# Optimization experiments

Measured on AMD Instinct MI355X. Metric: run time of the kernel, lower is better.

Reference implementation:

```python
import jax, jax.numpy as jnp
import numpy as np

B, S, H, NH = 2, 2048, 1024, 16
HD = H // NH  # 64


def setup_inputs() -> dict:
    key = jax.random.key(0)
    ks = jax.random.split(key, 9)
    s = 1.0 / np.sqrt(H)
    d = {"x": jax.random.normal(ks[0], (B, S, H), jnp.float32)}
    for i, n in enumerate(["Wq", "Wk", "Wv", "Wo"]):
        d[n] = jax.random.normal(ks[1 + i], (H, H), jnp.float32) * s
    for i, n in enumerate(["bq", "bk", "bv", "bo"]):
        d[n] = jax.random.normal(ks[5 + i], (H,), jnp.float32) * s
    return d


def _heads(x, W, b):
    # torch nn.Linear: y = x @ W.T + b, then split heads -> (B, NH, S, HD)
    y = x @ W.T + b
    return y.reshape(B, S, NH, HD).transpose(0, 2, 1, 3)


def _tetra_channels(t):
    # tetrapoint vector [a, 1-a, a*(1-a), clamp(1-(a+(1-a)),0,1)] for a scalar slice t
    a = jax.nn.sigmoid(t)
    na = 1.0 - a
    neither = jnp.clip(1.0 - (a + na), 0.0, 1.0)
    return jnp.stack([a, na, a * na, neither], axis=-1)  # (..., 4)


def reference(x, Wq, bq, Wk, bk, Wv, bv, Wo, bo):
    Q = _heads(x, Wq, bq)  # (B, NH, S, HD)
    K = _heads(x, Wk, bk)
    V = _heads(x, Wv, bv)
    # Original indexes Q_tetrapoints[:, :, :, 0] on [B,NH,S,HD,4]: selects head-dim
    # slot 0 (resp. 2) and keeps the 4 tetrapoint channels -> (B, NH, S, 4).
    Qa = _tetra_channels(Q[..., 0])
    Ka = _tetra_channels(K[..., 0])
    Qb = _tetra_channels(Q[..., 2])
    Kb = _tetra_channels(K[..., 2])
    scores = (jnp.einsum('bhsc,bhtc->bhst', Qa, Ka) / np.sqrt(HD)
              + 0.1 * jnp.einsum('bhsc,bhtc->bhst', Qb, Kb))  # (B, NH, S, S)
    w = jax.nn.softmax(scores, axis=-1)
    out = jnp.einsum('bhst,bhtd->bhsd', w, V)  # (B, NH, S, HD)
    out = out.transpose(0, 2, 1, 3).reshape(B, S, H)
    return out @ Wo.T + bo
```

## Files before the change

kernel.cpp:

```cpp
#include <hip/hip_runtime.h>
#include <hip/hip_bf16.h>

#define SS 2048
#define HH 1024
#define NHH 16
#define HDD 64

using f32x4  = __attribute__((ext_vector_type(4))) float;
using bf16x8 = __attribute__((ext_vector_type(8))) short;

__device__ __forceinline__ unsigned short f2bf(float f) {
    unsigned u = __builtin_bit_cast(unsigned, f);
    unsigned r = u + 0x7FFFu + ((u >> 16) & 1u);
    return (unsigned short)(r >> 16);
}

__device__ __forceinline__ unsigned bfround(float f) {
    unsigned u = __builtin_bit_cast(unsigned, f);
    return u + 0x7FFFu + ((u >> 16) & 1u);
}
__device__ __forceinline__ unsigned pack2bf(float a, float b) {
    return __builtin_amdgcn_perm(bfround(b), bfround(a), 0x07060302u);
}

__device__ __forceinline__ void tetra(float t, float* c) {
    float a = 1.f / (1.f + __expf(-t));
    float na = 1.f - a;
    float nei = 1.f - (a + na);
    nei = fminf(fmaxf(nei, 0.f), 1.f);
    c[0] = a; c[1] = na; c[2] = a * na; c[3] = nei;
}

__global__ __launch_bounds__(256) void cvt_kernel(
    const float* __restrict__ x, const float* __restrict__ Wv, const float* __restrict__ Wo,
    const float* __restrict__ Wq, const float* __restrict__ Wk,
    const float* __restrict__ bq, const float* __restrict__ bk,
    unsigned short* __restrict__ xb, unsigned short* __restrict__ Wvb, unsigned short* __restrict__ Wob,
    unsigned short* __restrict__ wselb, float* __restrict__ bselws)
{
    if (blockIdx.x >= 2048) {
        int n = blockIdx.x - 2048;
        int h = n >> 2, q = n & 3;
        int rowIdx = h * HDD + ((q & 1) ? 2 : 0);
        const float* src  = (q & 2) ? Wk : Wq;
        const float* bsrc = (q & 2) ? bk : bq;
        int t = threadIdx.x;
        float4 v = *(const float4*)(src + (size_t)rowIdx * HH + t * 4);
        uint2 pk;
        pk.x = pack2bf(v.x, v.y);
        pk.y = pack2bf(v.z, v.w);
        *(uint2*)(wselb + (size_t)n * HH + t * 4) = pk;
        if (t == 0) bselws[n] = bsrc[rowIdx];
        return;
    }
    size_t gid = (size_t)blockIdx.x * 256 + threadIdx.x;
    size_t base = gid * 8;
    {
        float4 a = *(const float4*)(x + base);
        float4 b = *(const float4*)(x + base + 4);
        uint4 pk;
        pk.x = pack2bf(a.x, a.y);
        pk.y = pack2bf(a.z, a.w);
        pk.z = pack2bf(b.x, b.y);
        pk.w = pack2bf(b.z, b.w);
        *(uint4*)(xb + base) = pk;
    }
    if (base < 1048576) {
        float4 a = *(const float4*)(Wv + base);
        float4 b = *(const float4*)(Wv + base + 4);
        uint4 pk;
        pk.x = pack2bf(a.x, a.y);
        pk.y = pack2bf(a.z, a.w);
        pk.z = pack2bf(b.x, b.y);
        pk.w = pack2bf(b.z, b.w);
        *(uint4*)(Wvb + base) = pk;
        a = *(const float4*)(Wo + base);
        b = *(const float4*)(Wo + base + 4);
        pk.x = pack2bf(a.x, a.y);
        pk.y = pack2bf(a.z, a.w);
        pk.z = pack2bf(b.x, b.y);
        pk.w = pack2bf(b.z, b.w);
        *(uint4*)(Wob + base) = pk;
    }
}

__global__ __launch_bounds__(256) void qk_gemm_kernel(
    const unsigned short* __restrict__ xb, const unsigned short* __restrict__ wselb,
    const float* __restrict__ bselws,
    unsigned short* __restrict__ qfb, unsigned short* __restrict__ kfb)
{
    __shared__ unsigned short xs[32][72];
    __shared__ unsigned short ws[64][72];
    __shared__ float ys[32][68];
    int tid = threadIdx.x;
    int wave = tid >> 6, lane = tid & 63;
    int l15 = lane & 15, l16 = lane >> 4;
    int m0 = blockIdx.x * 32;
    int n0w = wave * 16;

    int xr = tid >> 3, xseg = (tid & 7) * 8;
    int wr = tid >> 2, wseg = (tid & 3) * 16;
    const unsigned short* xp = xb + (size_t)(m0 + xr) * HH + xseg;
    const unsigned short* wp = wselb + (size_t)wr * HH + wseg;

    f32x4 acc[2] = {};

    uint4 xv  = *(const uint4*)(xp);
    uint4 wv0 = *(const uint4*)(wp);
    uint4 wv1 = *(const uint4*)(wp + 8);

    for (int k0 = 0; k0 < HH; k0 += 64) {
        __syncthreads();
        *(uint4*)&xs[xr][xseg] = xv;
        *(uint4*)&ws[wr][wseg]     = wv0;
        *(uint4*)&ws[wr][wseg + 8] = wv1;
        __syncthreads();

        int kn = (k0 + 64) & (HH - 1);
        uint4 nxv  = *(const uint4*)(xp + kn);
        uint4 nwv0 = *(const uint4*)(wp + kn);
        uint4 nwv1 = *(const uint4*)(wp + kn + 8);

        #pragma unroll
        for (int kk = 0; kk < 64; kk += 32) {
            bf16x8 bfr = *(const bf16x8*)&ws[n0w + l15][kk + l16 * 8];
            #pragma unroll
            for (int mi = 0; mi < 2; mi++) {
                bf16x8 af = *(const bf16x8*)&xs[mi * 16 + l15][kk + l16 * 8];
                acc[mi] = __builtin_amdgcn_mfma_f32_16x16x32_bf16(af, bfr, acc[mi], 0, 0, 0);
            }
        }
        xv = nxv; wv0 = nwv0; wv1 = nwv1;
    }

    float bias = bselws[n0w + l15];
    __syncthreads();
    #pragma unroll
    for (int mi = 0; mi < 2; mi++)
        #pragma unroll
        for (int r = 0; r < 4; r++)
            ys[mi * 16 + l16 * 4 + r][n0w + l15] = acc[mi][r] + bias;
    __syncthreads();

    #pragma unroll
    for (int pass = 0; pass < 2; pass++) {
        int ml = tid & 31;
        int h = (tid >> 5) + pass * 8;
        float4 y4 = *(const float4*)&ys[ml][h * 4];
        float qa[4], qb2[4], ka[4], kb2[4];
        tetra(y4.x, qa);
        tetra(y4.y, qb2);
        tetra(y4.z, ka);
        tetra(y4.w, kb2);
        int m = m0 + ml, b = m >> 11, s = m & 2047;
        size_t base = ((size_t)(b * NHH + h) * SS + s) * 8;
        uint4 qp, kp;
        qp.x = pack2bf(qa[0] * 0.125f, qa[1] * 0.125f);
        qp.y = pack2bf(qa[2] * 0.125f, qa[3] * 0.125f);
        qp.z = pack2bf(qb2[0] * 0.1f, qb2[1] * 0.1f);
        qp.w = pack2bf(qb2[2] * 0.1f, qb2[3] * 0.1f);
        kp.x = pack2bf(ka[0], ka[1]);
        kp.y = pack2bf(ka[2], ka[3]);
        kp.z = pack2bf(kb2[0], kb2[1]);
        kp.w = pack2bf(kb2[2], kb2[3]);
        *(uint4*)(qfb + base) = qp;
        *(uint4*)(kfb + base) = kp;
    }
}

template<int OUT_MODE>
__global__ __launch_bounds__(256) void gemm_mfma(
    const unsigned short* __restrict__ A, const unsigned short* __restrict__ Bw,
    const float* __restrict__ bias, void* __restrict__ Cout)
{
    __shared__ unsigned short As[128][72];
    __shared__ unsigned short Bs[64][72];
    int tid = threadIdx.x;
    int wave = tid >> 6, lane = tid & 63;
    int l15 = lane & 15, l16 = lane >> 4;
    int wm = wave >> 1, wn = wave & 1;
    int m0 = blockIdx.y * 128, n0 = blockIdx.x * 64;

    int ar = tid >> 1, aseg = (tid & 1) * 32;
    int br = tid >> 2, bseg = (tid & 3) * 16;
    const unsigned short* Ap = A + (size_t)(m0 + ar) * HH + aseg;
    const unsigned short* Bp = Bw + (size_t)(n0 + br) * HH + bseg;

    f32x4 acc[4][2] = {};

    uint4 a0 = *(const uint4*)(Ap);
    uint4 a1 = *(const uint4*)(Ap + 8);
    uint4 a2 = *(const uint4*)(Ap + 16);
    uint4 a3 = *(const uint4*)(Ap + 24);
    uint4 b0 = *(const uint4*)(Bp);
    uint4 b1 = *(const uint4*)(Bp + 8);

    for (int k0 = 0; k0 < HH; k0 += 64) {
        __syncthreads();
        *(uint4*)&As[ar][aseg]      = a0;
        *(uint4*)&As[ar][aseg + 8]  = a1;
        *(uint4*)&As[ar][aseg + 16] = a2;
        *(uint4*)&As[ar][aseg + 24] = a3;
        *(uint4*)&Bs[br][bseg]      = b0;
        *(uint4*)&Bs[br][bseg + 8]  = b1;
        __syncthreads();

        int kn = (k0 + 64) & (HH - 1);
        uint4 na0 = *(const uint4*)(Ap + kn);
        uint4 na1 = *(const uint4*)(Ap + kn + 8);
        uint4 na2 = *(const uint4*)(Ap + kn + 16);
        uint4 na3 = *(const uint4*)(Ap + kn + 24);
        uint4 nb0 = *(const uint4*)(Bp + kn);
        uint4 nb1 = *(const uint4*)(Bp + kn + 8);

        #pragma unroll
        for (int kk = 0; kk < 64; kk += 32) {
            bf16x8 af[4], bfr[2];
            #pragma unroll
            for (int mi = 0; mi < 4; mi++)
                af[mi] = *(const bf16x8*)&As[wm * 64 + mi * 16 + l15][kk + l16 * 8];
            #pragma unroll
            for (int ni = 0; ni < 2; ni++)
                bfr[ni] = *(const bf16x8*)&Bs[wn * 32 + ni * 16 + l15][kk + l16 * 8];
            #pragma unroll
            for (int mi = 0; mi < 4; mi++)
                #pragma unroll
                for (int ni = 0; ni < 2; ni++)
                    acc[mi][ni] = __builtin_amdgcn_mfma_f32_16x16x32_bf16(af[mi], bfr[ni], acc[mi][ni], 0, 0, 0);
        }
        a0 = na0; a1 = na1; a2 = na2; a3 = na3; b0 = nb0; b1 = nb1;
    }

    float bv[2];
    #pragma unroll
    for (int ni = 0; ni < 2; ni++)
        bv[ni] = bias[n0 + wn * 32 + ni * 16 + l15];

    #pragma unroll
    for (int mi = 0; mi < 4; mi++) {
        #pragma unroll
        for (int ni = 0; ni < 2; ni++) {
            int n = n0 + wn * 32 + ni * 16 + l15;
            if (OUT_MODE == 0) {
                #pragma unroll
                for (int r = 0; r < 4; r++) {
                    int m = m0 + wm * 64 + mi * 16 + l16 * 4 + r;
                    ((float*)Cout)[(size_t)m * HH + n] = acc[mi][ni][r] + bv[ni];
                }
            } else {
                int m = m0 + wm * 64 + mi * 16 + l16 * 4;
                int b = m >> 11, s = m & 2047;
                int h = n >> 6, d = n & 63;
                uint2 pk;
                pk.x = pack2bf(acc[mi][ni][0] + bv[ni], acc[mi][ni][1] + bv[ni]);
                pk.y = pack2bf(acc[mi][ni][2] + bv[ni], acc[mi][ni][3] + bv[ni]);
                *(uint2*)((unsigned short*)Cout + ((size_t)((b * NHH + h) * HDD + d)) * SS + s) = pk;
            }
        }
    }
}

__global__ __launch_bounds__(256) void attn_mfma(
    const unsigned short* __restrict__ qfb, const unsigned short* __restrict__ kfb,
    const unsigned short* __restrict__ Vt, unsigned short* __restrict__ attnb)
{
    __shared__ unsigned short vt[64][72];
    __shared__ unsigned short ps[4][16][72];

    int tid = threadIdx.x;
    int wave = tid >> 6, lane = tid & 63;
    int l15 = lane & 15, l16 = lane >> 4;
    int bh = blockIdx.y, b = bh >> 4, h = bh & 15;
    int s0 = blockIdx.x * 64 + wave * 16;

    bf16x8 bfq = {0,0,0,0,0,0,0,0};
    if (l16 == 0)
        bfq = *(const bf16x8*)(qfb + ((size_t)bh * SS + s0 + l15) * 8);

    const short oneb = 0x3F80;
    bf16x8 ones = {oneb,oneb,oneb,oneb,oneb,oneb,oneb,oneb};

    const unsigned short* kfA = kfb + ((size_t)bh * SS + l15) * 8;
    int vd = tid >> 2, vseg = (tid & 3) * 16;
    const unsigned short* vsrc = Vt + ((size_t)bh * HDD + vd) * SS + vseg;

    f32x4 acc[4] = {};
    f32x4 accl = {};

    uint4 sv0 = *(const uint4*)(vsrc);
    uint4 sv1 = *(const uint4*)(vsrc + 8);
    bf16x8 kfr[4];
    #pragma unroll
    for (int tb = 0; tb < 4; tb++)
        kfr[tb] = *(const bf16x8*)(kfA + (size_t)(tb * 16) * 8);

    for (int t0 = 0; t0 < SS; t0 += 64) {
        __syncthreads();
        *(uint4*)&vt[vd][vseg]     = sv0;
        *(uint4*)&vt[vd][vseg + 8] = sv1;
        __syncthreads();

        int tn = (t0 + 64) & (SS - 1);
        uint4 nv0 = *(const uint4*)(vsrc + tn);
        uint4 nv1 = *(const uint4*)(vsrc + tn + 8);
        bf16x8 nkf[4];
        #pragma unroll
        for (int tb = 0; tb < 4; tb++)
            nkf[tb] = *(const bf16x8*)(kfA + (size_t)(tn + tb * 16) * 8);

        #pragma unroll
        for (int tb = 0; tb < 4; tb++) {
            f32x4 sc = {};
            sc = __builtin_amdgcn_mfma_f32_16x16x32_bf16(kfr[tb], bfq, sc, 0, 0, 0);
            float p0 = __expf(sc[0]);
            float p1 = __expf(sc[1]);
            float p2 = __expf(sc[2]);
            float p3 = __expf(sc[3]);
            uint2 pw;
            pw.x = pack2bf(p0, p1);
            pw.y = pack2bf(p2, p3);
            *(uint2*)&ps[wave][l15][tb * 16 + l16 * 4] = pw;
        }

        #pragma unroll
        for (int tk = 0; tk < 2; tk++) {
            bf16x8 ap = *(const bf16x8*)&ps[wave][l15][tk * 32 + l16 * 8];
            accl = __builtin_amdgcn_mfma_f32_16x16x32_bf16(ap, ones, accl, 0, 0, 0);
            #pragma unroll
            for (int nd = 0; nd < 4; nd++) {
                bf16x8 bv = *(const bf16x8*)&vt[nd * 16 + l15][tk * 32 + l16 * 8];
                acc[nd] = __builtin_amdgcn_mfma_f32_16x16x32_bf16(ap, bv, acc[nd], 0, 0, 0);
            }
        }

        sv0 = nv0; sv1 = nv1;
        #pragma unroll
        for (int tb = 0; tb < 4; tb++) kfr[tb] = nkf[tb];
    }

    #pragma unroll
    for (int r = 0; r < 4; r++) {
        float linv = 1.f / accl[r];
        int q = s0 + l16 * 4 + r;
        size_t row = (size_t)(b * SS + q) * HH + h * HDD;
        #pragma unroll
        for (int nd = 0; nd < 4; nd++)
            attnb[row + nd * 16 + l15] = f2bf(acc[nd][r] * linv);
    }
}

extern "C" void kernel_launch(void* const* d_in, const int* in_sizes, int n_in,
                              void* d_out, int out_size, void* d_ws, size_t ws_size,
                              hipStream_t stream)
{
    const float* x  = (const float*)d_in[0];
    const float* Wq = (const float*)d_in[1];
    const float* Wk = (const float*)d_in[2];
    const float* Wv = (const float*)d_in[3];
    const float* Wo = (const float*)d_in[4];
    const float* bq = (const float*)d_in[5];
    const float* bk = (const float*)d_in[6];
    const float* bv = (const float*)d_in[7];
    const float* bo = (const float*)d_in[8];

    unsigned short* qfb   = (unsigned short*)d_ws;
    unsigned short* kfb   = qfb + 524288;
    unsigned short* xb    = kfb + 524288;
    unsigned short* attnb = xb;
    unsigned short* Wvb   = xb + 4194304;
    unsigned short* Wob   = Wvb + 1048576;
    unsigned short* Vt    = Wob + 1048576;
    unsigned short* wselb  = Vt + 4194304;
    float*          bselws = (float*)(wselb + 65536);

    cvt_kernel<<<2112, 256, 0, stream>>>(x, Wv, Wo, Wq, Wk, bq, bk, xb, Wvb, Wob, wselb, bselws);
    qk_gemm_kernel<<<128, 256, 0, stream>>>(xb, wselb, bselws, qfb, kfb);
    gemm_mfma<2><<<dim3(16, 32), 256, 0, stream>>>(xb, Wvb, bv, Vt);
    attn_mfma<<<dim3(32, 32), 256, 0, stream>>>(qfb, kfb, Vt, attnb);
    gemm_mfma<0><<<dim3(16, 32), 256, 0, stream>>>(attnb, Wob, bo, (float*)d_out);
}
```

Measured before the change: 185.2 us.

## Process two query tiles per wave in attention and use exp2 with prescaled Q

The attention block shrinks from four waves to two, and each wave now handles 32 query rows as two 16-row groups. Each K fragment and V tile read from shared memory is reused across both groups, which halves the K global loads and the V LDS reads per query. The Q scale factors are multiplied by log2(e) so the softmax can use the hardware exp2 instead of __expf. Register pressure rises and each block has fewer waves to hide latency.

```diff
diff --git a/kernel.cpp b/kernel.cpp
--- a/kernel.cpp
+++ b/kernel.cpp
@@ -8,6 +8,12 @@
 
 using f32x4  = __attribute__((ext_vector_type(4))) float;
 using bf16x8 = __attribute__((ext_vector_type(8))) short;
+
+#if __has_builtin(__builtin_amdgcn_exp2f)
+#define EXP2F __builtin_amdgcn_exp2f
+#else
+#define EXP2F exp2f
+#endif
 
 __device__ __forceinline__ unsigned short f2bf(float f) {
     unsigned u = __builtin_bit_cast(unsigned, f);
@@ -154,11 +160,13 @@
         tetra(y4.w, kb2);
         int m = m0 + ml, b = m >> 11, s = m & 2047;
         size_t base = ((size_t)(b * NHH + h) * SS + s) * 8;
+        const float sA = 0.18033688011112042f;
+        const float sB = 0.14426950408889634f;
         uint4 qp, kp;
-        qp.x = pack2bf(qa[0] * 0.125f, qa[1] * 0.125f);
-        qp.y = pack2bf(qa[2] * 0.125f, qa[3] * 0.125f);
-        qp.z = pack2bf(qb2[0] * 0.1f, qb2[1] * 0.1f);
-        qp.w = pack2bf(qb2[2] * 0.1f, qb2[3] * 0.1f);
+        qp.x = pack2bf(qa[0] * sA, qa[1] * sA);
+        qp.y = pack2bf(qa[2] * sA, qa[3] * sA);
+        qp.z = pack2bf(qb2[0] * sB, qb2[1] * sB);
+        qp.w = pack2bf(qb2[2] * sB, qb2[3] * sB);
         kp.x = pack2bf(ka[0], ka[1]);
         kp.y = pack2bf(ka[2], ka[3]);
         kp.z = pack2bf(kb2[0], kb2[1]);
@@ -260,35 +268,39 @@
     }
 }
 
-__global__ __launch_bounds__(256) void attn_mfma(
+__global__ __launch_bounds__(128) void attn_mfma(
     const unsigned short* __restrict__ qfb, const unsigned short* __restrict__ kfb,
     const unsigned short* __restrict__ Vt, unsigned short* __restrict__ attnb)
 {
     __shared__ unsigned short vt[64][72];
-    __shared__ unsigned short ps[4][16][72];
+    __shared__ unsigned short ps[2][32][72];
 
     int tid = threadIdx.x;
     int wave = tid >> 6, lane = tid & 63;
     int l15 = lane & 15, l16 = lane >> 4;
     int bh = blockIdx.y, b = bh >> 4, h = bh & 15;
-    int s0 = blockIdx.x * 64 + wave * 16;
-
-    bf16x8 bfq = {0,0,0,0,0,0,0,0};
-    if (l16 == 0)
-        bfq = *(const bf16x8*)(qfb + ((size_t)bh * SS + s0 + l15) * 8);
+    int s0 = blockIdx.x * 64 + wave * 32;
+
+    bf16x8 bfq0 = {0,0,0,0,0,0,0,0};
+    bf16x8 bfq1 = {0,0,0,0,0,0,0,0};
+    if (l16 == 0) {
+        bfq0 = *(const bf16x8*)(qfb + ((size_t)bh * SS + s0 + l15) * 8);
+        bfq1 = *(const bf16x8*)(qfb + ((size_t)bh * SS + s0 + 16 + l15) * 8);
+    }
 
     const short oneb = 0x3F80;
     bf16x8 ones = {oneb,oneb,oneb,oneb,oneb,oneb,oneb,oneb};
 
     const unsigned short* kfA = kfb + ((size_t)bh * SS + l15) * 8;
-    int vd = tid >> 2, vseg = (tid & 3) * 16;
+    int vd = tid >> 1, vseg = (tid & 1) * 32;
     const unsigned short* vsrc = Vt + ((size_t)bh * HDD + vd) * SS + vseg;
 
-    f32x4 acc[4] = {};
-    f32x4 accl = {};
-
-    uint4 sv0 = *(const uint4*)(vsrc);
-    uint4 sv1 = *(const uint4*)(vsrc + 8);
+    f32x4 acc[2][4] = {};
+    f32x4 accl[2] = {};
+
+    uint4 sv[4];
+    #pragma unroll
+    for (int j = 0; j < 4; j++) sv[j] = *(const uint4*)(vsrc + j * 8);
     bf16x8 kfr[4];
     #pragma unroll
     for (int tb = 0; tb < 4; tb++)
@@ -296,13 +308,15 @@
 
     for (int t0 = 0; t0 < SS; t0 += 64) {
         __syncthreads();
-        *(uint4*)&vt[vd][vseg]     = sv0;
-        *(uint4*)&vt[vd][vseg + 8] = sv1;
+        #pragma unroll
+        for (int j = 0; j < 4; j++)
+            *(uint4*)&vt[vd][vseg + j * 8] = sv[j];
         __syncthreads();
 
         int tn = (t0 + 64) & (SS - 1);
-        uint4 nv0 = *(const uint4*)(vsrc + tn);
-        uint4 nv1 = *(const uint4*)(vsrc + tn + 8);
+        uint4 nv[4];
+        #pragma unroll
+        for (int j = 0; j < 4; j++) nv[j] = *(const uint4*)(vsrc + tn + j * 8);
         bf16x8 nkf[4];
         #pragma unroll
         for (int tb = 0; tb < 4; tb++)
@@ -310,42 +324,55 @@
 
         #pragma unroll
         for (int tb = 0; tb < 4; tb++) {
-            f32x4 sc = {};
-            sc = __builtin_amdgcn_mfma_f32_16x16x32_bf16(kfr[tb], bfq, sc, 0, 0, 0);
-            float p0 = __expf(sc[0]);
-            float p1 = __expf(sc[1]);
-            float p2 = __expf(sc[2]);
-            float p3 = __expf(sc[3]);
-            uint2 pw;
-            pw.x = pack2bf(p0, p1);
-            pw.y = pack2bf(p2, p3);
-            *(uint2*)&ps[wave][l15][tb * 16 + l16 * 4] = pw;
+            #pragma unroll
+            for (int qg = 0; qg < 2; qg++) {
+                f32x4 sc = {};
+                sc = __builtin_amdgcn_mfma_f32_16x16x32_bf16(kfr[tb], qg ? bfq1 : bfq0, sc, 0, 0, 0);
+                float p0 = EXP2F(sc[0]);
+                float p1 = EXP2F(sc[1]);
+                float p2 = EXP2F(sc[2]);
+                float p3 = EXP2F(sc[3]);
+                uint2 pw;
+                pw.x = pack2bf(p0, p1);
+                pw.y = pack2bf(p2, p3);
+                *(uint2*)&ps[wave][qg * 16 + l15][tb * 16 + l16 * 4] = pw;
+            }
         }
 
         #pragma unroll
         for (int tk = 0; tk < 2; tk++) {
-            bf16x8 ap = *(const bf16x8*)&ps[wave][l15][tk * 32 + l16 * 8];
-            accl = __builtin_amdgcn_mfma_f32_16x16x32_bf16(ap, ones, accl, 0, 0, 0);
+            bf16x8 ap[2];
+            #pragma unroll
+            for (int qg = 0; qg < 2; qg++) {
+                ap[qg] = *(const bf16x8*)&ps[wave][qg * 16 + l15][tk * 32 + l16 * 8];
+                accl[qg] = __builtin_amdgcn_mfma_f32_16x16x32_bf16(ap[qg], ones, accl[qg], 0, 0, 0);
+            }
             #pragma unroll
             for (int nd = 0; nd < 4; nd++) {
                 bf16x8 bv = *(const bf16x8*)&vt[nd * 16 + l15][tk * 32 + l16 * 8];
-                acc[nd] = __builtin_amdgcn_mfma_f32_16x16x32_bf16(ap, bv, acc[nd], 0, 0, 0);
+                #pragma unroll
+                for (int qg = 0; qg < 2; qg++)
+                    acc[qg][nd] = __builtin_amdgcn_mfma_f32_16x16x32_bf16(ap[qg], bv, acc[qg][nd], 0, 0, 0);
             }
         }
 
-        sv0 = nv0; sv1 = nv1;
+        #pragma unroll
+        for (int j = 0; j < 4; j++) sv[j] = nv[j];
         #pragma unroll
         for (int tb = 0; tb < 4; tb++) kfr[tb] = nkf[tb];
     }
 
     #pragma unroll
-    for (int r = 0; r < 4; r++) {
-        float linv = 1.f / accl[r];
-        int q = s0 + l16 * 4 + r;
-        size_t row = (size_t)(b * SS + q) * HH + h * HDD;
-        #pragma unroll
-        for (int nd = 0; nd < 4; nd++)
-            attnb[row + nd * 16 + l15] = f2bf(acc[nd][r] * linv);
+    for (int qg = 0; qg < 2; qg++) {
+        #pragma unroll
+        for (int r = 0; r < 4; r++) {
+            float linv = 1.f / accl[qg][r];
+            int q = s0 + qg * 16 + l16 * 4 + r;
+            size_t row = (size_t)(b * SS + q) * HH + h * HDD;
+            #pragma unroll
+            for (int nd = 0; nd < 4; nd++)
+                attnb[row + nd * 16 + l15] = f2bf(acc[qg][nd][r] * linv);
+        }
     }
 }
 
@@ -376,6 +403,6 @@
     cvt_kernel<<<2112, 256, 0, stream>>>(x, Wv, Wo, Wq, Wk, bq, bk, xb, Wvb, Wob, wselb, bselws);
     qk_gemm_kernel<<<128, 256, 0, stream>>>(xb, wselb, bselws, qfb, kfb);
     gemm_mfma<2><<<dim3(16, 32), 256, 0, stream>>>(xb, Wvb, bv, Vt);
-    attn_mfma<<<dim3(32, 32), 256, 0, stream>>>(qfb, kfb, Vt, attnb);
+    attn_mfma<<<dim3(32, 32), 128, 0, stream>>>(qfb, kfb, Vt, attnb);
     gemm_mfma<0><<<dim3(16, 32), 256, 0, stream>>>(attnb, Wob, bo, (float*)d_out);
 }
```

Measured after the change: 220.7 us. +19.1%, slower.
